# Performance work log

Hardware: AMD Instinct MI355X
Metric: run time of the kernel (lower is better)

Reference implementation:

```python
import math
import jax, jax.numpy as jnp
import numpy as np

B = 2
N = 48           # max_atoms
A = 16           # num_atom_types
E = 5            # num_bond_types
HID = 384
NH = 8
HD = HID // NH   # 48
LYR = 4
MLP = 4 * HID
L = N + N * N    # 2352 sequence length (nodes + flattened edges)


def setup_inputs() -> dict:
    key = jax.random.key(0)
    ks = iter(jax.random.split(key, 48))
    r = lambda *s: jax.random.normal(next(ks), s, jnp.float32) * 0.02
    d = {
        "x": jax.random.normal(next(ks), (B, N, A), jnp.float32),
        "adj": jax.random.normal(next(ks), (B, N, N, E), jnp.float32),
        "t": jax.random.uniform(next(ks), (B,), jnp.float32),
        # embeddings
        "node_w": r(A, HID), "node_b": jnp.zeros((HID,), jnp.float32),
        "edge_w": r(E, HID), "edge_b": jnp.zeros((HID,), jnp.float32),
        "pos": r(L, HID),
        # timestep MLP (SinusoidalPositionalEmbedding(HID) -> Linear(HID,4H) -> SiLU -> Linear(4H,H))
        "t_w1": r(HID, 4 * HID), "t_b1": jnp.zeros((4 * HID,), jnp.float32),
        "t_w2": r(4 * HID, HID), "t_b2": jnp.zeros((HID,), jnp.float32),
        # stacked per-layer params
        "ada1_w": r(LYR, HID, 2 * HID), "ada1_b": jnp.zeros((LYR, 2 * HID), jnp.float32),
        "ada2_w": r(LYR, HID, 2 * HID), "ada2_b": jnp.zeros((LYR, 2 * HID), jnp.float32),
        "q_w": r(LYR, HID, HID), "q_b": jnp.zeros((LYR, HID), jnp.float32),
        "k_w": r(LYR, HID, HID), "k_b": jnp.zeros((LYR, HID), jnp.float32),
        "v_w": r(LYR, HID, HID), "v_b": jnp.zeros((LYR, HID), jnp.float32),
        "o_w": r(LYR, HID, HID), "o_b": jnp.zeros((LYR, HID), jnp.float32),
        "m1_w": r(LYR, HID, MLP), "m1_b": jnp.zeros((LYR, MLP), jnp.float32),
        "m2_w": r(LYR, MLP, HID), "m2_b": jnp.zeros((LYR, HID), jnp.float32),
        # final norm + heads (heads random instead of zero-init so output is informative)
        "fn_g": jnp.ones((HID,), jnp.float32), "fn_b": jnp.zeros((HID,), jnp.float32),
        "on_w": r(HID, A), "on_b": jnp.zeros((A,), jnp.float32),
        "oe_w": r(HID, E), "oe_b": jnp.zeros((E,), jnp.float32),
    }
    return d


def _ln(z):
    # LayerNorm(elementwise_affine=False), eps=1e-5
    mu = z.mean(-1, keepdims=True)
    var = z.var(-1, keepdims=True)
    return (z - mu) * jax.lax.rsqrt(var + 1e-5)


def _forward(x, adj, t, node_w, node_b, edge_w, edge_b, pos,
             t_w1, t_b1, t_w2, t_b2,
             ada1_w, ada1_b, ada2_w, ada2_b,
             q_w, q_b, k_w, k_b, v_w, v_b, o_w, o_b,
             m1_w, m1_b, m2_w, m2_b,
             fn_g, fn_b, on_w, on_b, oe_w, oe_b):
    b = x.shape[0]
    # embed nodes and edges, concat into sequence [b, L, HID]
    h_nodes = x @ node_w + node_b                       # [b, N, H]
    h_edges = adj.reshape(b, N * N, E) @ edge_w + edge_b  # [b, N*N, H]
    h = jnp.concatenate([h_nodes, h_edges], axis=1) + pos[None]
    # sinusoidal timestep embedding -> cond [b, HID]
    half = HID // 2
    freqs = jnp.exp(-math.log(10000.0) * jnp.arange(half, dtype=jnp.float32) / half)
    ang = t[:, None].astype(jnp.float32) * freqs[None, :]
    temb = jnp.concatenate([jnp.sin(ang), jnp.cos(ang)], axis=-1)
    cond = jax.nn.silu(temb @ t_w1 + t_b1) @ t_w2 + t_b2
    inv_scale = 1.0 / math.sqrt(HD)
    for i in range(LYR):
        # AdaLN 1 + attention
        sc, sh = jnp.split(cond @ ada1_w[i] + ada1_b[i], 2, axis=-1)
        n = _ln(h) * (1.0 + sc[:, None, :]) + sh[:, None, :]
        q = (n @ q_w[i] + q_b[i]).reshape(b, L, NH, HD)
        k = (n @ k_w[i] + k_b[i]).reshape(b, L, NH, HD)
        v = (n @ v_w[i] + v_b[i]).reshape(b, L, NH, HD)
        scores = jnp.einsum('bqhd,bkhd->bhqk', q, k) * inv_scale
        attn = jax.nn.softmax(scores, axis=-1)
        ao = jnp.einsum('bhqk,bkhd->bqhd', attn, v).reshape(b, L, HID)
        h = h + ao @ o_w[i] + o_b[i]
        # AdaLN 2 + MLP (exact GELU as in nn.GELU default)
        sc2, sh2 = jnp.split(cond @ ada2_w[i] + ada2_b[i], 2, axis=-1)
        n2 = _ln(h) * (1.0 + sc2[:, None, :]) + sh2[:, None, :]
        h = h + jax.nn.gelu(n2 @ m1_w[i] + m1_b[i], approximate=False) @ m2_w[i] + m2_b[i]
    h = _ln(h) * fn_g + fn_b
    node_out = h[:, :N] @ on_w + on_b                   # [b, N, A]
    edge_out = (h[:, N:] @ oe_w + oe_b).reshape(b, N, N, E)
    return node_out, edge_out


def reference(x, adj, t, node_w, node_b, edge_w, edge_b, pos,
              t_w1, t_b1, t_w2, t_b2,
              ada1_w, ada1_b, ada2_w, ada2_b,
              q_w, q_b, k_w, k_b, v_w, v_b, o_w, o_b,
              m1_w, m1_b, m2_w, m2_b,
              fn_g, fn_b, on_w, on_b, oe_w, oe_b):
    return _forward(x, adj, t, node_w, node_b, edge_w, edge_b, pos,
                    t_w1, t_b1, t_w2, t_b2,
                    ada1_w, ada1_b, ada2_w, ada2_b,
                    q_w, q_b, k_w, k_b, v_w, v_b, o_w, o_b,
                    m1_w, m1_b, m2_w, m2_b,
                    fn_g, fn_b, on_w, on_b, oe_w, oe_b)
```

## Files before the change

### kernel.cpp

```cpp
#include <hip/hip_runtime.h>
#include <hip/hip_bf16.h>
#include <math.h>

typedef __hip_bfloat16 bf16;
typedef __attribute__((ext_vector_type(8))) short short8;
typedef __attribute__((ext_vector_type(4))) float f32x4;

#define B_ 2
#define N_ 48
#define A_ 16
#define E_ 5
#define HID 384
#define NHD 8
#define HD 48
#define LYR 4
#define MLPD 1536
#define L_ 2352
#define M_ 4704
#define VLP 2432
#define QSCALE 0.20823513f

#define WQ_  0LL
#define WK_  589824LL
#define WV_  1179648LL
#define WO_  1769472LL
#define WM1_ 2359296LL
#define WM2_ 4718592LL
#define WTOT 7077888
#define BQ_  0
#define BK_  1536
#define BV_  3072
#define BO_  4608
#define BM1_ 6144
#define BM2_ 12288
#define BTOT 13824

#define GLOAD16(gp, lp) __builtin_amdgcn_global_load_lds( \
    (const __attribute__((address_space(1))) unsigned int*)(gp), \
    (__attribute__((address_space(3))) unsigned int*)(lp), 16, 0, 0)

static __device__ __forceinline__ float b2f(bf16 v) { return __bfloat162float(v); }
static __device__ __forceinline__ float us2f(unsigned short u) {
    return __uint_as_float(((unsigned)u) << 16);
}
static __device__ __forceinline__ unsigned short f2us(float f) {
    bf16 h = __float2bfloat16(f);
    return *reinterpret_cast<unsigned short*>(&h);
}
static __device__ __forceinline__ float ldv(const float* p, size_t i) { return p[i]; }
static __device__ __forceinline__ float ldv(const bf16*  p, size_t i) { return b2f(p[i]); }
static __device__ __forceinline__ void  stv(float* p, size_t i, float v) { p[i] = v; }
static __device__ __forceinline__ void  stv(bf16*  p, size_t i, float v) { p[i] = __float2bfloat16(v); }
static __device__ __forceinline__ float4 ld4(const float* p, size_t i) {
    return *reinterpret_cast<const float4*>(p + i);
}
static __device__ __forceinline__ float4 ld4(const bf16* p, size_t i) {
    ushort4 u = *reinterpret_cast<const ushort4*>(p + i);
    return make_float4(us2f(u.x), us2f(u.y), us2f(u.z), us2f(u.w));
}

__global__ void k_detect(const void* w, int* flag) {
    if (threadIdx.x == 0 && blockIdx.x == 0) {
        const bf16* p = (const bf16*)w;
        int isf = 0;
        for (int i = 0; i < 256; ++i) {
            float v = fabsf(b2f(p[i]));
            if (!(v <= 1000.0f)) { isf = 1; break; }
        }
        *flag = isf;
    }
}

template <typename T>
static __device__ void prepw_body(
    const T* q_w, const T* k_w, const T* v_w, const T* o_w,
    const T* m1_w, const T* m2_w, bf16* wbt)
{
    __shared__ unsigned short Ts[64][72];
    const int z = blockIdx.y;
    const int kind = z >> 2, l = z & 3;
    const T* src; int K, N; long long dbase;
    switch (kind) {
        case 0: src = q_w;  K = 384;  N = 384;  dbase = WQ_;  break;
        case 1: src = k_w;  K = 384;  N = 384;  dbase = WK_;  break;
        case 2: src = v_w;  K = 384;  N = 384;  dbase = WV_;  break;
        case 3: src = o_w;  K = 384;  N = 384;  dbase = WO_;  break;
        case 4: src = m1_w; K = 384;  N = 1536; dbase = WM1_; break;
        default: src = m2_w; K = 1536; N = 384; dbase = WM2_; break;
    }
    const int Nt = N >> 6;
    const int tiles = (K >> 6) * Nt;
    if (blockIdx.x >= tiles) return;
    const int tk = blockIdx.x / Nt, tn = blockIdx.x % Nt;
    const int k0 = tk*64, n0 = tn*64;
    const size_t soff = (size_t)l * K * N;
    const size_t doff = (size_t)dbase + (size_t)l * K * N;
    const int tid = threadIdx.x;
    {
        const int kk = tid >> 2, nc = (tid & 3) * 16;
        #pragma unroll
        for (int j = 0; j < 16; ++j)
            Ts[kk][nc + j] = f2us(ldv(src, soff + (size_t)(k0 + kk)*N + n0 + nc + j));
    }
    __syncthreads();
    {
        const int nn = tid >> 2, kc = (tid & 3) * 16;
        unsigned short tmp[16];
        #pragma unroll
        for (int j = 0; j < 16; ++j) tmp[j] = Ts[kc + j][nn];
        unsigned short* dst = (unsigned short*)wbt + doff + (size_t)(n0 + nn)*K + k0 + kc;
        *reinterpret_cast<short8*>(dst)     = *reinterpret_cast<short8*>(&tmp[0]);
        *reinterpret_cast<short8*>(dst + 8) = *reinterpret_cast<short8*>(&tmp[8]);
    }
}

__global__ __launch_bounds__(256) void k_prepw(
    const void* q_w, const void* k_w, const void* v_w, const void* o_w,
    const void* m1_w, const void* m2_w, const int* __restrict__ fl, bf16* __restrict__ wbt)
{
    if (*fl) prepw_body<float>((const float*)q_w, (const float*)k_w, (const float*)v_w,
                               (const float*)o_w, (const float*)m1_w, (const float*)m2_w, wbt);
    else     prepw_body<bf16>((const bf16*)q_w, (const bf16*)k_w, (const bf16*)v_w,
                              (const bf16*)o_w, (const bf16*)m1_w, (const bf16*)m2_w, wbt);
}

template <typename T>
static __device__ void prepb_body(
    const T* q_b, const T* k_b, const T* v_b, const T* o_b,
    const T* m1_b, const T* m2_b, bf16* bb)
{
    for (int i = threadIdx.x; i < BTOT; i += 256) {
        float v;
        if      (i < BK_)  v = ldv(q_b,  i);
        else if (i < BV_)  v = ldv(k_b,  i - BK_);
        else if (i < BO_)  v = ldv(v_b,  i - BV_);
        else if (i < BM1_) v = ldv(o_b,  i - BO_);
        else if (i < BM2_) v = ldv(m1_b, i - BM1_);
        else               v = ldv(m2_b, i - BM2_);
        bb[i] = __float2bfloat16(v);
    }
}

__global__ __launch_bounds__(256) void k_prepb(
    const void* q_b, const void* k_b, const void* v_b, const void* o_b,
    const void* m1_b, const void* m2_b, const int* __restrict__ fl, bf16* __restrict__ bb)
{
    if (*fl) prepb_body<float>((const float*)q_b, (const float*)k_b, (const float*)v_b,
                               (const float*)o_b, (const float*)m1_b, (const float*)m2_b, bb);
    else     prepb_body<bf16>((const bf16*)q_b, (const bf16*)k_b, (const bf16*)v_b,
                              (const bf16*)o_b, (const bf16*)m1_b, (const bf16*)m2_b, bb);
}

template <typename T>
static __device__ void embed_body(
    const T* x, const T* adj, const T* node_w, const T* node_b,
    const T* edge_w, const T* edge_b, const T* pos, float* h)
{
    const int bl = blockIdx.x;
    const int b = bl / L_, l = bl % L_;
    const int c = threadIdx.x;
    float acc;
    if (l < N_) {
        acc = ldv(node_b, c);
        const size_t xr = (size_t)(b*N_ + l)*A_;
        #pragma unroll
        for (int a = 0; a < A_; ++a) acc += ldv(x, xr + a) * ldv(node_w, (size_t)a*HID + c);
    } else {
        const int e = l - N_;
        acc = ldv(edge_b, c);
        const size_t ar = ((size_t)b*N_*N_ + e)*E_;
        #pragma unroll
        for (int j = 0; j < E_; ++j) acc += ldv(adj, ar + j) * ldv(edge_w, (size_t)j*HID + c);
    }
    h[(size_t)bl*HID + c] = acc + ldv(pos, (size_t)l*HID + c);
}

__global__ __launch_bounds__(384) void k_embed(
    const void* x, const void* adj, const void* node_w, const void* node_b,
    const void* edge_w, const void* edge_b, const void* pos,
    const int* __restrict__ fl, float* __restrict__ h)
{
    if (*fl) embed_body<float>((const float*)x, (const float*)adj, (const float*)node_w,
                               (const float*)node_b, (const float*)edge_w, (const float*)edge_b,
                               (const float*)pos, h);
    else     embed_body<bf16>((const bf16*)x, (const bf16*)adj, (const bf16*)node_w,
                              (const bf16*)node_b, (const bf16*)edge_w, (const bf16*)edge_b,
                              (const bf16*)pos, h);
}

template <typename T>
static __device__ void cond1_body(const T* t, const T* t_w1, const T* t_b1, float* hid)
{
    __shared__ float temb[HID];
    __shared__ float red[4][64];
    const int b = blockIdx.x, jb = blockIdx.y, tid = threadIdx.x;
    const float tv = ldv(t, b);
    for (int c = tid; c < HID; c += 256) {
        int i = (c < 192) ? c : c - 192;
        float f = expf(-9.2103403719761836f * (float)i / 192.0f);
        float ang = tv * f;
        temb[c] = (c < 192) ? sinf(ang) : cosf(ang);
    }
    __syncthreads();
    const int ko = tid >> 6, jo = tid & 63;
    const int j = jb*64 + jo;
    float acc = 0.f;
    for (int i = ko*96; i < (ko + 1)*96; ++i)
        acc += temb[i] * ldv(t_w1, (size_t)i*4*HID + j);
    red[ko][jo] = acc;
    __syncthreads();
    if (ko == 0) {
        float a = red[0][jo] + red[1][jo] + red[2][jo] + red[3][jo] + ldv(t_b1, j);
        hid[(size_t)b*4*HID + j] = a / (1.0f + expf(-a));
    }
}

__global__ __launch_bounds__(256) void k_cond1(
    const void* t, const void* t_w1, const void* t_b1,
    const int* __restrict__ fl, float* __restrict__ hid)
{
    if (*fl) cond1_body<float>((const float*)t, (const float*)t_w1, (const float*)t_b1, hid);
    else     cond1_body<bf16>((const bf16*)t, (const bf16*)t_w1, (const bf16*)t_b1, hid);
}

template <typename T>
static __device__ void cond2_body(const T* t_w2, const T* t_b2, const float* hid, float* part)
{
    __shared__ float hs[128];
    const int b = blockIdx.x, ch = blockIdx.y, c = threadIdx.x;
    const int j0 = ch*128;
    if (c < 128) hs[c] = hid[(size_t)b*4*HID + j0 + c];
    __syncthreads();
    float acc = (ch == 0) ? ldv(t_b2, c) : 0.f;
    for (int jj = 0; jj < 128; ++jj)
        acc += hs[jj] * ldv(t_w2, (size_t)(j0 + jj)*HID + c);
    part[((size_t)b*12 + ch)*HID + c] = acc;
}

__global__ __launch_bounds__(384) void k_cond2(
    const void* t_w2, const void* t_b2, const int* __restrict__ fl,
    const float* __restrict__ hid, float* __restrict__ part)
{
    if (*fl) cond2_body<float>((const float*)t_w2, (const float*)t_b2, hid, part);
    else     cond2_body<bf16>((const bf16*)t_w2, (const bf16*)t_b2, hid, part);
}

template <typename T>
static __device__ void cond3_body(
    const T* ada1_w, const T* ada1_b, const T* ada2_w, const T* ada2_b,
    const float* part, float* ada_out)
{
    __shared__ float cs[HID];
    const int slot = blockIdx.x / 3, ob = blockIdx.x % 3, b = blockIdx.y;
    const int tid = threadIdx.x;
    for (int c = tid; c < HID; c += 256) {
        float s = 0.f;
        #pragma unroll
        for (int ch = 0; ch < 12; ++ch) s += part[((size_t)b*12 + ch)*HID + c];
        cs[c] = s;
    }
    __syncthreads();
    const int layer = slot >> 1, which = slot & 1;
    const int o = ob*256 + tid;
    const T* W  = which ? ada2_w : ada1_w;
    const T* Bi = which ? ada2_b : ada1_b;
    float acc = ldv(Bi, (size_t)layer*768 + o);
    const size_t wb = (size_t)layer*HID*768 + o;
    for (int c = 0; c < HID; ++c) acc += cs[c] * ldv(W, wb + (size_t)c*768);
    ada_out[((size_t)slot*B_ + b)*768 + o] = acc;
}

__global__ __launch_bounds__(256) void k_cond3(
    const void* ada1_w, const void* ada1_b, const void* ada2_w, const void* ada2_b,
    const int* __restrict__ fl, const float* __restrict__ part, float* __restrict__ ada_out)
{
    if (*fl) cond3_body<float>((const float*)ada1_w, (const float*)ada1_b,
                               (const float*)ada2_w, (const float*)ada2_b, part, ada_out);
    else     cond3_body<bf16>((const bf16*)ada1_w, (const bf16*)ada1_b,
                              (const bf16*)ada2_w, (const bf16*)ada2_b, part, ada_out);
}

__global__ __launch_bounds__(256) void k_adaln(
    const float* __restrict__ h, const float* __restrict__ ada,
    bf16* __restrict__ n, int slot)
{
    const int row  = blockIdx.x * 4 + (threadIdx.x >> 6);
    const int lane = threadIdx.x & 63;
    const int b = row / L_;
    const float* hr = h + (size_t)row*HID;
    float v[6]; float s = 0.f, ss = 0.f;
    #pragma unroll
    for (int j = 0; j < 6; ++j) { float t = hr[lane + j*64]; v[j] = t; s += t; ss += t*t; }
    #pragma unroll
    for (int off = 32; off; off >>= 1) { s += __shfl_xor(s, off); ss += __shfl_xor(ss, off); }
    const float mu = s * (1.0f/HID);
    const float rs = rsqrtf(fmaxf(ss * (1.0f/HID) - mu*mu, 0.0f) + 1e-5f);
    const float* ap = ada + ((size_t)slot*B_ + b)*768;
    bf16* nr = n + (size_t)row*HID;
    #pragma unroll
    for (int j = 0; j < 6; ++j) {
        int c = lane + j*64;
        nr[c] = __float2bfloat16((v[j] - mu)*rs*(1.0f + ap[c]) + ap[384 + c]);
    }
}

static __device__ __forceinline__ void gemm_epilogue(
    f32x4 (&acc)[2][2], float bcol0, float bcol1,
    bf16* Cb, float* Cf, int M, int N, int act, int mode,
    int bm, int bn, int wm, int wn, int quad, int c)
{
    const float bcol[2] = {bcol0, bcol1};
    #pragma unroll
    for (int mi = 0; mi < 2; ++mi)
        #pragma unroll
        for (int ni = 0; ni < 2; ++ni) {
            const int col = bn + wn*32 + ni*16 + c;
            #pragma unroll
            for (int r = 0; r < 4; ++r) {
                const int row = bm + wm*32 + mi*16 + quad*4 + r;
                if (row < M) {
                    float v = acc[mi][ni][r] + bcol[ni];
                    if (act) v = 0.5f * v * (1.0f + erff(v * 0.70710678118654752f));
                    if (mode == 1) Cf[(size_t)row*N + col] += v;
                    else if (mode == 0) Cb[(size_t)row*N + col] = __float2bfloat16(v);
                    else if (mode == 3) Cb[(size_t)row*N + col] = __float2bfloat16(v * QSCALE);
                    else {
                        const int b   = row >= L_ ? 1 : 0;
                        const int key = row - b*L_;
                        const int hh  = col / 48, d = col - hh*48;
                        Cb[((size_t)(b*8 + hh)*48 + d)*VLP + key] = __float2bfloat16(v);
                    }
                }
            }
        }
}

template <typename T>
static __device__ void gemm_body(
    const bf16* A, const T* W, long long woff, const T* bias, long long boff,
    bf16* Cb, float* Cf, int M, int N, int K, int act, int mode)
{
    __shared__ __align__(16) unsigned short As[64][72];
    __shared__ __align__(16) unsigned short Bt[64][72];
    const int tid  = threadIdx.x;
    const int wv   = tid >> 6, lane = tid & 63;
    const int quad = lane >> 4, c = lane & 15;
    const int wm = wv & 1, wn = wv >> 1;
    const int bm = blockIdx.x * 64, bn = blockIdx.y * 64;
    const int arow = tid >> 3, ach = tid & 7;
    f32x4 acc[2][2] = {{{0.f,0.f,0.f,0.f},{0.f,0.f,0.f,0.f}},
                       {{0.f,0.f,0.f,0.f},{0.f,0.f,0.f,0.f}}};
    for (int k0 = 0; k0 < K; k0 += 64) {
        short8 av[2]; float4 w0[2], w1[2];
        #pragma unroll
        for (int i = 0; i < 2; ++i) {
            const int row = i*32 + arow;
            av[i] = short8{0,0,0,0,0,0,0,0};
            if (bm + row < M)
                av[i] = *reinterpret_cast<const short8*>(
                            A + (size_t)(bm + row)*K + k0 + ach*8);
            const size_t wrow = (size_t)woff + (size_t)(k0 + i*32 + arow)*N + bn + ach*8;
            w0[i] = ld4(W, wrow);
            w1[i] = ld4(W, wrow + 4);
        }
        __syncthreads();
        #pragma unroll
        for (int i = 0; i < 2; ++i) {
            *reinterpret_cast<short8*>(&As[i*32 + arow][ach*8]) = av[i];
            const int kk = i*32 + arow, nb0 = ach*8;
            Bt[nb0+0][kk] = f2us(w0[i].x); Bt[nb0+1][kk] = f2us(w0[i].y);
            Bt[nb0+2][kk] = f2us(w0[i].z); Bt[nb0+3][kk] = f2us(w0[i].w);
            Bt[nb0+4][kk] = f2us(w1[i].x); Bt[nb0+5][kk] = f2us(w1[i].y);
            Bt[nb0+6][kk] = f2us(w1[i].z); Bt[nb0+7][kk] = f2us(w1[i].w);
        }
        __syncthreads();
        #pragma unroll
        for (int ks = 0; ks < 2; ++ks) {
            short8 af[2], bfr[2];
            #pragma unroll
            for (int mi = 0; mi < 2; ++mi)
                af[mi] = *reinterpret_cast<const short8*>(
                             &As[wm*32 + mi*16 + c][ks*32 + quad*8]);
            #pragma unroll
            for (int ni = 0; ni < 2; ++ni)
                bfr[ni] = *reinterpret_cast<const short8*>(
                              &Bt[wn*32 + ni*16 + c][ks*32 + quad*8]);
            #pragma unroll
            for (int mi = 0; mi < 2; ++mi)
                #pragma unroll
                for (int ni = 0; ni < 2; ++ni)
                    acc[mi][ni] = __builtin_amdgcn_mfma_f32_16x16x32_bf16(
                                      af[mi], bfr[ni], acc[mi][ni], 0, 0, 0);
        }
    }
    gemm_epilogue(acc, ldv(bias, (size_t)boff + bn + wn*32 + c),
                  ldv(bias, (size_t)boff + bn + wn*32 + 16 + c),
                  Cb, Cf, M, N, act, mode, bm, bn, wm, wn, quad, c);
}

__global__ __launch_bounds__(256) void k_gemm(
    const bf16* __restrict__ A, const void* W, long long woff, const void* bias, long long boff,
    bf16* Cb, float* Cf, int M, int N, int K, int act, int mode,
    const int* __restrict__ fl)
{
    if (*fl) gemm_body<float>(A, (const float*)W, woff, (const float*)bias, boff,
                              Cb, Cf, M, N, K, act, mode);
    else     gemm_body<bf16>(A, (const bf16*)W, woff, (const bf16*)bias, boff,
                             Cb, Cf, M, N, K, act, mode);
}

__global__ __launch_bounds__(256) void k_gemm_qkv(
    const bf16* __restrict__ A,
    const void* qw, const void* kw, const void* vw,
    const void* qb, const void* kb, const void* vb,
    long long woff, long long boff,
    bf16* Cq, bf16* Ck, bf16* Cv, const int* __restrict__ fl)
{
    const int z = blockIdx.z;
    const void* W  = (z == 0) ? qw : (z == 1) ? kw : vw;
    const void* Bi = (z == 0) ? qb : (z == 1) ? kb : vb;
    bf16* C        = (z == 0) ? Cq : (z == 1) ? Ck : Cv;
    const int mode = (z == 0) ? 3 : (z == 2) ? 2 : 0;
    if (*fl) gemm_body<float>(A, (const float*)W, woff, (const float*)Bi, boff,
                              C, nullptr, M_, HID, HID, 0, mode);
    else     gemm_body<bf16>(A, (const bf16*)W, woff, (const bf16*)Bi, boff,
                             C, nullptr, M_, HID, HID, 0, mode);
}

static __device__ void gemm_t_body(
    const bf16* A, const bf16* Wt, long long woff, const bf16* bias, long long boff,
    bf16* Cb, float* Cf, int M, int N, int K, int act, int mode)
{
    __shared__ __align__(16) unsigned short Tz[2][2][4096];
    const int tid  = threadIdx.x;
    const int wv   = tid >> 6, lane = tid & 63;
    const int quad = lane >> 4, c = lane & 15;
    const int wm = wv & 1, wn = wv >> 1;
    const int bm = blockIdx.x * 64, bn = blockIdx.y * 64;
    const unsigned short* Ag = (const unsigned short*)A;
    const unsigned short* Wg = (const unsigned short*)Wt + woff;
    const int sr = tid >> 3;
    const int csw0 = (((tid & 7) ^ (sr & 7)) << 3);
    int ar0 = bm + sr;        ar0 = ar0 < M ? ar0 : M - 1;
    int ar1 = bm + 32 + sr;   ar1 = ar1 < M ? ar1 : M - 1;
    const int wr0 = bn + sr, wr1 = bn + 32 + sr;
    const int ldso = tid * 8;

    f32x4 acc[2][2] = {{{0.f,0.f,0.f,0.f},{0.f,0.f,0.f,0.f}},
                       {{0.f,0.f,0.f,0.f},{0.f,0.f,0.f,0.f}}};

    #define STAGE_T(buf, k0) do { \
        GLOAD16(Ag + (size_t)ar0*K + (k0) + csw0, &Tz[buf][0][ldso]); \
        GLOAD16(Ag + (size_t)ar1*K + (k0) + csw0, &Tz[buf][0][2048 + ldso]); \
        GLOAD16(Wg + (size_t)wr0*K + (k0) + csw0, &Tz[buf][1][ldso]); \
        GLOAD16(Wg + (size_t)wr1*K + (k0) + csw0, &Tz[buf][1][2048 + ldso]); \
    } while (0)

    STAGE_T(0, 0);
    __syncthreads();
    int cur = 0;
    for (int k0 = 0; k0 < K; k0 += 64) {
        if (k0 + 64 < K) STAGE_T(cur ^ 1, k0 + 64);
        #pragma unroll
        for (int ks = 0; ks < 2; ++ks) {
            short8 af[2], bfr[2];
            #pragma unroll
            for (int mi = 0; mi < 2; ++mi) {
                const int row = wm*32 + mi*16 + c;
                const char* p = (const char*)&Tz[cur][0][0]
                              + (row*128 + (((ks*64 + quad*16)) ^ ((row & 7) << 4)));
                af[mi] = *reinterpret_cast<const short8*>(p);
            }
            #pragma unroll
            for (int ni = 0; ni < 2; ++ni) {
                const int row = wn*32 + ni*16 + c;
                const char* p = (const char*)&Tz[cur][1][0]
                              + (row*128 + (((ks*64 + quad*16)) ^ ((row & 7) << 4)));
                bfr[ni] = *reinterpret_cast<const short8*>(p);
            }
            #pragma unroll
            for (int mi = 0; mi < 2; ++mi)
                #pragma unroll
                for (int ni = 0; ni < 2; ++ni)
                    acc[mi][ni] = __builtin_amdgcn_mfma_f32_16x16x32_bf16(
                                      af[mi], bfr[ni], acc[mi][ni], 0, 0, 0);
        }
        __syncthreads();
        cur ^= 1;
    }
    #undef STAGE_T
    gemm_epilogue(acc, b2f(bias[boff + bn + wn*32 + c]),
                  b2f(bias[boff + bn + wn*32 + 16 + c]),
                  Cb, Cf, M, N, act, mode, bm, bn, wm, wn, quad, c);
}

__global__ __launch_bounds__(256) void k_gemm_t(
    const bf16* __restrict__ A, const bf16* __restrict__ Wt, long long woff,
    const bf16* __restrict__ bias, long long boff,
    bf16* Cb, float* Cf, int M, int N, int K, int act, int mode)
{
    gemm_t_body(A, Wt, woff, bias, boff, Cb, Cf, M, N, K, act, mode);
}

__global__ __launch_bounds__(256) void k_gemm_qkv_t(
    const bf16* __restrict__ A, const bf16* __restrict__ wbt, const bf16* __restrict__ bb,
    int lyr, bf16* Cq, bf16* Ck, bf16* Cv)
{
    const int z = blockIdx.z;
    long long woff; long long boff; bf16* C; int mode;
    if (z == 0)      { woff = WQ_ + (long long)lyr*147456; boff = BQ_ + lyr*384; C = Cq; mode = 3; }
    else if (z == 1) { woff = WK_ + (long long)lyr*147456; boff = BK_ + lyr*384; C = Ck; mode = 0; }
    else             { woff = WV_ + (long long)lyr*147456; boff = BV_ + lyr*384; C = Cv; mode = 2; }
    gemm_t_body(A, wbt, woff, bb, boff, C, nullptr, M_, HID, HID, 0, mode);
}

__global__ __launch_bounds__(512) void k_attn(
    const bf16* __restrict__ q, const bf16* __restrict__ k,
    const bf16* __restrict__ vt, bf16* __restrict__ ao)
{
    __shared__ __align__(16) unsigned short Ks[2][64][80];
    __shared__ __align__(16) unsigned short Vt[2][48][72];
    __shared__ __align__(16) unsigned short Pq[8][16][72];
    const int tid  = threadIdx.x;
    const int w    = tid >> 6, lane = tid & 63;
    const int quad = lane >> 4, c = lane & 15;
    const int qt = w & 3, sp = w >> 2;
    const int bh = blockIdx.y;
    const size_t base  = (size_t)(bh >> 3)*L_*HID + (size_t)(bh & 7)*HD;
    const size_t vbase = (size_t)bh*48*VLP;
    const int q0 = blockIdx.x*64 + qt*16;
    const bool qvalid = q0 < L_;
    const int qrow = qvalid ? (q0 + c) : c;

    short8 qf0, qf1;
    {
        const unsigned short* qp = (const unsigned short*)(q + base + (size_t)qrow*HID);
        qf0 = *reinterpret_cast<const short8*>(qp + quad*8);
        if (quad < 2) qf1 = *reinterpret_cast<const short8*>(qp + 32 + quad*8);
        else          qf1 = short8{0,0,0,0,0,0,0,0};
    }
    f32x4 o0 = {0.f,0.f,0.f,0.f}, o1 = {0.f,0.f,0.f,0.f}, o2 = {0.f,0.f,0.f,0.f};
    float m = -3.0e38f, lsum = 0.f;

    const int t256 = tid & 255, grp = tid >> 8;
    const int krow0 = t256 >> 3, kch = t256 & 7;
    const int krow1 = 32 + krow0;
    const int vd0 = krow0;
    const int vd1 = 32 + (krow0 & 15);
    const bool vl1 = (t256 < 128);
    const unsigned short* kq = (const unsigned short*)(k + base);
    const unsigned short* vq = (const unsigned short*)(vt + vbase);
    const short8 Z8 = short8{0,0,0,0,0,0,0,0};
    short8 kr0 = Z8, kr1 = Z8, vr0, vr1 = Z8;
    {
        const int kb0 = grp*1216;
        if (kch < 6) {
            kr0 = *reinterpret_cast<const short8*>(kq + (size_t)(kb0 + krow0)*HID + kch*8);
            kr1 = *reinterpret_cast<const short8*>(kq + (size_t)(kb0 + krow1)*HID + kch*8);
        }
        vr0 = *reinterpret_cast<const short8*>(vq + (size_t)vd0*VLP + kb0 + kch*8);
        if (vl1) vr1 = *reinterpret_cast<const short8*>(vq + (size_t)vd1*VLP + kb0 + kch*8);
    }

    for (int tt = 0; tt < 19; ++tt) {
        __syncthreads();
        *reinterpret_cast<short8*>(&Ks[grp][krow0][kch*8]) = kr0;
        *reinterpret_cast<short8*>(&Ks[grp][krow1][kch*8]) = kr1;
        *reinterpret_cast<short8*>(&Vt[grp][vd0][kch*8])   = vr0;
        if (vl1) *reinterpret_cast<short8*>(&Vt[grp][vd1][kch*8]) = vr1;
        __syncthreads();
        if (tt < 18) {
            const int nb0 = grp*1216 + (tt + 1)*64;
            if (kch < 6) {
                kr0 = *reinterpret_cast<const short8*>(kq + (size_t)(nb0 + krow0)*HID + kch*8);
                kr1 = *reinterpret_cast<const short8*>(kq + (size_t)(nb0 + krow1)*HID + kch*8);
            }
            vr0 = *reinterpret_cast<const short8*>(vq + (size_t)vd0*VLP + nb0 + kch*8);
            if (vl1) vr1 = *reinterpret_cast<const short8*>(vq + (size_t)vd1*VLP + nb0 + kch*8);
        }

        const int kt = sp*1216 + tt*64;
        float sv[16];
        #pragma unroll
        for (int t = 0; t < 4; ++t) {
            f32x4 acc = {0.f,0.f,0.f,0.f};
            short8 a0 = *reinterpret_cast<const short8*>(&Ks[sp][t*16 + c][quad*8]);
            short8 a1 = *reinterpret_cast<const short8*>(&Ks[sp][t*16 + c][32 + quad*8]);
            acc = __builtin_amdgcn_mfma_f32_16x16x32_bf16(a0, qf0, acc, 0, 0, 0);
            acc = __builtin_amdgcn_mfma_f32_16x16x32_bf16(a1, qf1, acc, 0, 0, 0);
            #pragma unroll
            for (int r = 0; r < 4; ++r) sv[t*4 + r] = acc[r];
        }
        if (sp == 1 && tt >= 17) {
            #pragma unroll
            for (int t = 0; t < 4; ++t)
                #pragma unroll
                for (int r = 0; r < 4; ++r)
                    if (kt + t*16 + quad*4 + r >= L_) sv[t*4 + r] = -3.0e38f;
        }
        float tmax = fmaxf(fmaxf(fmaxf(sv[0], sv[1]),  fmaxf(sv[2],  sv[3])),
                           fmaxf(fmaxf(sv[4], sv[5]),  fmaxf(sv[6],  sv[7])));
        float tmx2 = fmaxf(fmaxf(fmaxf(sv[8], sv[9]),  fmaxf(sv[10], sv[11])),
                           fmaxf(fmaxf(sv[12], sv[13]), fmaxf(sv[14], sv[15])));
        tmax = fmaxf(tmax, tmx2);
        tmax = fmaxf(tmax, __shfl_xor(tmax, 16));
        tmax = fmaxf(tmax, __shfl_xor(tmax, 32));
        if (!__all(tmax <= m + 8.0f)) {
            const float mn = fmaxf(m, tmax);
            const float alpha = exp2f(m - mn);
            m = mn;
            lsum *= alpha;
            o0 *= alpha; o1 *= alpha; o2 *= alpha;
        }
        float psum = 0.f;
        unsigned short pv[16];
        #pragma unroll
        for (int i = 0; i < 16; ++i) {
            const float p = exp2f(sv[i] - m);
            psum += p;
            pv[i] = f2us(p);
        }
        lsum += psum;
        #pragma unroll
        for (int t = 0; t < 4; ++t)
            *reinterpret_cast<ushort4*>(&Pq[w][c][t*16 + quad*4]) =
                make_ushort4(pv[t*4+0], pv[t*4+1], pv[t*4+2], pv[t*4+3]);
        #pragma unroll
        for (int s = 0; s < 2; ++s) {
            short8 pf  = *reinterpret_cast<const short8*>(&Pq[w][c][s*32 + quad*8]);
            short8 vf0 = *reinterpret_cast<const short8*>(&Vt[sp][c][s*32 + quad*8]);
            short8 vf1 = *reinterpret_cast<const short8*>(&Vt[sp][16 + c][s*32 + quad*8]);
            short8 vf2 = *reinterpret_cast<const short8*>(&Vt[sp][32 + c][s*32 + quad*8]);
            o0 = __builtin_amdgcn_mfma_f32_16x16x32_bf16(vf0, pf, o0, 0, 0, 0);
            o1 = __builtin_amdgcn_mfma_f32_16x16x32_bf16(vf1, pf, o1, 0, 0, 0);
            o2 = __builtin_amdgcn_mfma_f32_16x16x32_bf16(vf2, pf, o2, 0, 0, 0);
        }
    }
    float lw = lsum;
    lw += __shfl_xor(lw, 16);
    lw += __shfl_xor(lw, 32);
    float* Mg = (float*)&Ks[0][0][0];
    __syncthreads();
    if (sp == 1) {
        float* dst = Mg + (size_t)(qt*64 + lane)*14;
        dst[0] = o0[0]; dst[1] = o0[1]; dst[2]  = o0[2]; dst[3]  = o0[3];
        dst[4] = o1[0]; dst[5] = o1[1]; dst[6]  = o1[2]; dst[7]  = o1[3];
        dst[8] = o2[0]; dst[9] = o2[1]; dst[10] = o2[2]; dst[11] = o2[3];
        dst[12] = m; dst[13] = lw;
    }
    __syncthreads();
    if (sp == 0 && qvalid) {
        const float* src = Mg + (size_t)(qt*64 + lane)*14;
        const float m2 = src[12], l2 = src[13];
        const float mm = fmaxf(m, m2);
        const float a1 = exp2f(m - mm), a2 = exp2f(m2 - mm);
        const float inv = 1.0f / (lw*a1 + l2*a2);
        unsigned short* orow = (unsigned short*)(ao + base + (size_t)(q0 + c)*HID);
        const f32x4 ot[3] = {o0, o1, o2};
        #pragma unroll
        for (int dt = 0; dt < 3; ++dt) {
            ushort4 w4;
            w4.x = f2us((ot[dt][0]*a1 + src[dt*4+0]*a2) * inv);
            w4.y = f2us((ot[dt][1]*a1 + src[dt*4+1]*a2) * inv);
            w4.z = f2us((ot[dt][2]*a1 + src[dt*4+2]*a2) * inv);
            w4.w = f2us((ot[dt][3]*a1 + src[dt*4+3]*a2) * inv);
            *reinterpret_cast<ushort4*>(orow + dt*16 + quad*4) = w4;
        }
    }
}

template <typename T, typename TO>
static __device__ void final_body(
    const float* h, const T* fn_g, const T* fn_b,
    const T* on_w, const T* on_b, const T* oe_w, const T* oe_b, TO* out)
{
    __shared__ float hf[HID];
    const int row = blockIdx.x;
    const int b = row / L_, l = row % L_;
    const int lane = threadIdx.x;
    const float* hr = h + (size_t)row*HID;
    float v[6]; float s = 0.f, ss = 0.f;
    #pragma unroll
    for (int j = 0; j < 6; ++j) { float t = hr[lane + j*64]; v[j] = t; s += t; ss += t*t; }
    #pragma unroll
    for (int off = 32; off; off >>= 1) { s += __shfl_xor(s, off); ss += __shfl_xor(ss, off); }
    const float mu = s * (1.0f/HID);
    const float rs = rsqrtf(fmaxf(ss * (1.0f/HID) - mu*mu, 0.0f) + 1e-5f);
    #pragma unroll
    for (int j = 0; j < 6; ++j) {
        int c = lane + j*64;
        hf[c] = (v[j] - mu) * rs * ldv(fn_g, c) + ldv(fn_b, c);
    }
    __syncthreads();
    if (l < N_) {
        if (lane < A_) {
            float acc = ldv(on_b, lane);
            for (int c = 0; c < HID; ++c) acc += hf[c] * ldv(on_w, (size_t)c*A_ + lane);
            stv(out, (size_t)(b*N_ + l)*A_ + lane, acc);
        }
    } else {
        const int e = l - N_;
        if (lane < E_) {
            float acc = ldv(oe_b, lane);
            for (int c = 0; c < HID; ++c) acc += hf[c] * ldv(oe_w, (size_t)c*E_ + lane);
            stv(out, (size_t)B_*N_*A_ + ((size_t)b*N_*N_ + e)*E_ + lane, acc);
        }
    }
}

__global__ __launch_bounds__(64) void k_final(
    const float* __restrict__ h, const void* fn_g, const void* fn_b,
    const void* on_w, const void* on_b, const void* oe_w, const void* oe_b,
    const int* __restrict__ fl, void* out)
{
    if (*fl) final_body<float, float>(h, (const float*)fn_g, (const float*)fn_b,
                                      (const float*)on_w, (const float*)on_b,
                                      (const float*)oe_w, (const float*)oe_b, (float*)out);
    else     final_body<bf16, bf16>(h, (const bf16*)fn_g, (const bf16*)fn_b,
                                    (const bf16*)on_w, (const bf16*)on_b,
                                    (const bf16*)oe_w, (const bf16*)oe_b, (bf16*)out);
}

extern "C" void kernel_launch(void* const* d_in, const int* in_sizes, int n_in,
                              void* d_out, int out_size, void* d_ws, size_t ws_size,
                              hipStream_t stream) {
    const void* x      = d_in[0];
    const void* adj    = d_in[1];
    const void* t      = d_in[2];
    const void* node_w = d_in[3];
    const void* node_b = d_in[4];
    const void* edge_w = d_in[5];
    const void* edge_b = d_in[6];
    const void* pos    = d_in[7];
    const void* t_w1   = d_in[8];
    const void* t_b1   = d_in[9];
    const void* t_w2   = d_in[10];
    const void* t_b2   = d_in[11];
    const void* ada1_w = d_in[12];
    const void* ada1_b = d_in[13];
    const void* ada2_w = d_in[14];
    const void* ada2_b = d_in[15];
    const void* q_w    = d_in[16];
    const void* q_b    = d_in[17];
    const void* k_w    = d_in[18];
    const void* k_b    = d_in[19];
    const void* v_w    = d_in[20];
    const void* v_b    = d_in[21];
    const void* o_w    = d_in[22];
    const void* o_b    = d_in[23];
    const void* m1_w   = d_in[24];
    const void* m1_b   = d_in[25];
    const void* m2_w   = d_in[26];
    const void* m2_b   = d_in[27];
    const void* fn_g   = d_in[28];
    const void* fn_b   = d_in[29];
    const void* on_w   = d_in[30];
    const void* on_b   = d_in[31];
    const void* oe_w   = d_in[32];
    const void* oe_b   = d_in[33];

    const size_t SZ  = (size_t)M_ * HID;
    const size_t VTZ = (size_t)B_*NHD*HD*VLP;
    const size_t FLT = SZ + 12288 + (size_t)B_*4*HID + (size_t)B_*12*HID;
    const size_t M1FULL = (size_t)M_ * MLPD;
    const size_t BF_BASE = 3*SZ + VTZ;
    const size_t BF_BIG  = SZ + M1FULL;
    const size_t NEED      = 256 + sizeof(float)*FLT + sizeof(bf16)*BF_BASE;
    const size_t NEED_BIG  = 256 + sizeof(float)*FLT + sizeof(bf16)*BF_BIG;
    const size_t NEED_PREP = 256 + sizeof(float)*FLT
                           + sizeof(bf16)*(BF_BIG + WTOT + BTOT);
    if (ws_size < NEED) {
        hipMemsetAsync(d_out, 0, (size_t)out_size*sizeof(bf16), stream);
        return;
    }
    const bool big  = (ws_size >= NEED_BIG);
    const bool prep = (ws_size >= NEED_PREP);
    int*   fl   = (int*)d_ws;
    float* h    = (float*)((char*)d_ws + 256);
    float* ada  = h + SZ;
    float* hid  = ada + 12288;
    float* part = hid + (size_t)B_*4*HID;
    bf16* nb  = (bf16*)(part + (size_t)B_*12*HID);
    bf16* qb  = nb + SZ;
    bf16* kb  = qb + SZ;
    bf16* vtb = kb + SZ;
    bf16* m1c = kb;
    bf16* m1f = qb;
    bf16* wbt = nb + BF_BIG;
    bf16* bb  = wbt + WTOT;

    k_detect<<<1, 64, 0, stream>>>(node_w, fl);
    if (prep) {
        k_prepw<<<dim3(144, 24), 256, 0, stream>>>(q_w, k_w, v_w, o_w, m1_w, m2_w, fl, wbt);
        k_prepb<<<1, 256, 0, stream>>>(q_b, k_b, v_b, o_b, m1_b, m2_b, fl, bb);
    }
    k_embed<<<M_, HID, 0, stream>>>(x, adj, node_w, node_b, edge_w, edge_b, pos, fl, h);
    k_cond1<<<dim3(B_, 24), 256, 0, stream>>>(t, t_w1, t_b1, fl, hid);
    k_cond2<<<dim3(B_, 12), 384, 0, stream>>>(t_w2, t_b2, fl, hid, part);
    k_cond3<<<dim3(24, B_), 256, 0, stream>>>(ada1_w, ada1_b, ada2_w, ada2_b, fl, part, ada);
    for (int i = 0; i < LYR; ++i) {
        const long long woff   = (long long)i * HID * HID;
        const long long boff   = (long long)i * HID;
        const long long m1woff = (long long)i * HID * MLPD;
        const long long m1boff = (long long)i * MLPD;
        const long long m2woff = (long long)i * MLPD * HID;

        k_adaln<<<M_/4, 256, 0, stream>>>(h, ada, nb, 2*i);
        if (prep) {
            k_gemm_qkv_t<<<dim3(74, 6, 3), 256, 0, stream>>>(nb, wbt, bb, i, qb, kb, vtb);
            k_attn<<<dim3(37, B_*NHD), 512, 0, stream>>>(qb, kb, vtb, nb);
            k_gemm_t<<<dim3(74, 6), 256, 0, stream>>>(nb, wbt, WO_ + (long long)i*147456,
                                                      bb, BO_ + i*384,
                                                      nullptr, h, M_, HID, HID, 0, 1);
            k_adaln<<<M_/4, 256, 0, stream>>>(h, ada, nb, 2*i + 1);
            k_gemm_t<<<dim3(74, 24), 256, 0, stream>>>(nb, wbt, WM1_ + (long long)i*589824,
                                                       bb, BM1_ + i*MLPD,
                                                       m1f, nullptr, M_, MLPD, HID, 1, 0);
            k_gemm_t<<<dim3(74, 6), 256, 0, stream>>>(m1f, wbt, WM2_ + (long long)i*589824,
                                                      bb, BM2_ + i*384,
                                                      nullptr, h, M_, HID, MLPD, 0, 1);
        } else {
            k_gemm_qkv<<<dim3(74, 6, 3), 256, 0, stream>>>(nb, q_w, k_w, v_w, q_b, k_b, v_b,
                                                           woff, boff, qb, kb, vtb, fl);
            k_attn<<<dim3(37, B_*NHD), 512, 0, stream>>>(qb, kb, vtb, nb);
            k_gemm<<<dim3(74, 6), 256, 0, stream>>>(nb, o_w, woff, o_b, boff,
                                                    nullptr, h, M_, HID, HID, 0, 1, fl);
            k_adaln<<<M_/4, 256, 0, stream>>>(h, ada, nb, 2*i + 1);
            if (big) {
                k_gemm<<<dim3(74, 24), 256, 0, stream>>>(nb, m1_w, m1woff, m1_b, m1boff,
                                                         m1f, nullptr, M_, MLPD, HID, 1, 0, fl);
                k_gemm<<<dim3(74, 6), 256, 0, stream>>>(m1f, m2_w, m2woff, m2_b, boff,
                                                        nullptr, h, M_, HID, MLPD, 0, 1, fl);
            } else {
                for (int c = 0; c < 2; ++c) {
                    k_gemm<<<dim3(37, 24), 256, 0, stream>>>(nb + (size_t)c*2352*HID,
                                                             m1_w, m1woff, m1_b, m1boff,
                                                             m1c, nullptr, 2352, MLPD, HID, 1, 0, fl);
                    k_gemm<<<dim3(37, 6), 256, 0, stream>>>(m1c, m2_w, m2woff, m2_b, boff,
                                                            nullptr, h + (size_t)c*2352*HID,
                                                            2352, HID, MLPD, 0, 1, fl);
                }
            }
        }
    }
    k_final<<<M_, 64, 0, stream>>>(h, fn_g, fn_b, on_w, on_b, oe_w, oe_b, fl, (void*)d_out);
}
```

Measured before the change: 818.1 us.

## Split attention keys across two blocks with flash-decoding style merge kernel

Adds a split-K attention kernel where each block handles half of the key sequence with 256 threads, writing normalized partial outputs plus max/sum stats to workspace, and a separate merge kernel that combines the two halves. This replaces the in-block two-wave split with grid-level splitting, doubling block count for better CU occupancy. It costs extra global writes/reads of partials and an extra kernel launch, and only runs if the workspace is large enough.

```diff
diff --git a/kernel.cpp b/kernel.cpp
--- a/kernel.cpp
+++ b/kernel.cpp
@@ -34,6 +34,9 @@
 #define BM1_ 6144
 #define BM2_ 12288
 #define BTOT 13824
+
+#define PO_E  ((size_t)16*2368*2*48)
+#define PML_E ((size_t)16*2368*2*2)
 
 #define GLOAD16(gp, lp) __builtin_amdgcn_global_load_lds( \
     (const __attribute__((address_space(1))) unsigned int*)(gp), \
@@ -666,6 +669,174 @@
             w4.w = f2us((ot[dt][3]*a1 + src[dt*4+3]*a2) * inv);
             *reinterpret_cast<ushort4*>(orow + dt*16 + quad*4) = w4;
         }
+    }
+}
+
+__global__ __launch_bounds__(256) void k_attn_fd(
+    const bf16* __restrict__ q, const bf16* __restrict__ k,
+    const bf16* __restrict__ vt, bf16* __restrict__ pob, float* __restrict__ pml)
+{
+    __shared__ __align__(16) unsigned short Ks[64][80];
+    __shared__ __align__(16) unsigned short Vt[48][72];
+    __shared__ __align__(16) unsigned short Pq[4][16][72];
+    const int tid  = threadIdx.x;
+    const int w    = tid >> 6, lane = tid & 63;
+    const int quad = lane >> 4, c = lane & 15;
+    const int bh   = blockIdx.y;
+    const int half = blockIdx.z;
+    const size_t base  = (size_t)(bh >> 3)*L_*HID + (size_t)(bh & 7)*HD;
+    const size_t vbase = (size_t)bh*48*VLP;
+    const int q0 = blockIdx.x*64 + w*16;
+    const bool qvalid = q0 < L_;
+    const int qrow = qvalid ? (q0 + c) : c;
+
+    short8 qf0, qf1;
+    {
+        const unsigned short* qp = (const unsigned short*)(q + base + (size_t)qrow*HID);
+        qf0 = *reinterpret_cast<const short8*>(qp + quad*8);
+        if (quad < 2) qf1 = *reinterpret_cast<const short8*>(qp + 32 + quad*8);
+        else          qf1 = short8{0,0,0,0,0,0,0,0};
+    }
+    f32x4 o0 = {0.f,0.f,0.f,0.f}, o1 = {0.f,0.f,0.f,0.f}, o2 = {0.f,0.f,0.f,0.f};
+    float m = -3.0e38f, lsum = 0.f;
+
+    const int krow0 = tid >> 3, kch = tid & 7;
+    const int krow1 = 32 + krow0;
+    const int vd0 = krow0;
+    const int vd1 = 32 + (krow0 & 15);
+    const bool vl1 = (tid < 128);
+    const unsigned short* kq = (const unsigned short*)(k + base);
+    const unsigned short* vq = (const unsigned short*)(vt + vbase);
+    const short8 Z8 = short8{0,0,0,0,0,0,0,0};
+    short8 kr0 = Z8, kr1 = Z8, vr0, vr1 = Z8;
+    const int kbase = half*1216;
+    {
+        if (kch < 6) {
+            kr0 = *reinterpret_cast<const short8*>(kq + (size_t)(kbase + krow0)*HID + kch*8);
+            kr1 = *reinterpret_cast<const short8*>(kq + (size_t)(kbase + krow1)*HID + kch*8);
+        }
+        vr0 = *reinterpret_cast<const short8*>(vq + (size_t)vd0*VLP + kbase + kch*8);
+        if (vl1) vr1 = *reinterpret_cast<const short8*>(vq + (size_t)vd1*VLP + kbase + kch*8);
+    }
+
+    for (int tt = 0; tt < 19; ++tt) {
+        __syncthreads();
+        *reinterpret_cast<short8*>(&Ks[krow0][kch*8]) = kr0;
+        *reinterpret_cast<short8*>(&Ks[krow1][kch*8]) = kr1;
+        *reinterpret_cast<short8*>(&Vt[vd0][kch*8])   = vr0;
+        if (vl1) *reinterpret_cast<short8*>(&Vt[vd1][kch*8]) = vr1;
+        __syncthreads();
+        if (tt < 18) {
+            const int nb0 = kbase + (tt + 1)*64;
+            if (kch < 6) {
+                kr0 = *reinterpret_cast<const short8*>(kq + (size_t)(nb0 + krow0)*HID + kch*8);
+                kr1 = *reinterpret_cast<const short8*>(kq + (size_t)(nb0 + krow1)*HID + kch*8);
+            }
+            vr0 = *reinterpret_cast<const short8*>(vq + (size_t)vd0*VLP + nb0 + kch*8);
+            if (vl1) vr1 = *reinterpret_cast<const short8*>(vq + (size_t)vd1*VLP + nb0 + kch*8);
+        }
+
+        const int kt = kbase + tt*64;
+        float sv[16];
+        #pragma unroll
+        for (int t = 0; t < 4; ++t) {
+            f32x4 acc = {0.f,0.f,0.f,0.f};
+            short8 a0 = *reinterpret_cast<const short8*>(&Ks[t*16 + c][quad*8]);
+            short8 a1 = *reinterpret_cast<const short8*>(&Ks[t*16 + c][32 + quad*8]);
+            acc = __builtin_amdgcn_mfma_f32_16x16x32_bf16(a0, qf0, acc, 0, 0, 0);
+            acc = __builtin_amdgcn_mfma_f32_16x16x32_bf16(a1, qf1, acc, 0, 0, 0);
+            #pragma unroll
+            for (int r = 0; r < 4; ++r) sv[t*4 + r] = acc[r];
+        }
+        if (half == 1 && tt >= 17) {
+            #pragma unroll
+            for (int t = 0; t < 4; ++t)
+                #pragma unroll
+                for (int r = 0; r < 4; ++r)
+                    if (kt + t*16 + quad*4 + r >= L_) sv[t*4 + r] = -3.0e38f;
+        }
+        float tmax = fmaxf(fmaxf(fmaxf(sv[0], sv[1]),  fmaxf(sv[2],  sv[3])),
+                           fmaxf(fmaxf(sv[4], sv[5]),  fmaxf(sv[6],  sv[7])));
+        float tmx2 = fmaxf(fmaxf(fmaxf(sv[8], sv[9]),  fmaxf(sv[10], sv[11])),
+                           fmaxf(fmaxf(sv[12], sv[13]), fmaxf(sv[14], sv[15])));
+        tmax = fmaxf(tmax, tmx2);
+        tmax = fmaxf(tmax, __shfl_xor(tmax, 16));
+        tmax = fmaxf(tmax, __shfl_xor(tmax, 32));
+        if (!__all(tmax <= m + 8.0f)) {
+            const float mn = fmaxf(m, tmax);
+            const float alpha = exp2f(m - mn);
+            m = mn;
+            lsum *= alpha;
+            o0 *= alpha; o1 *= alpha; o2 *= alpha;
+        }
+        float psum = 0.f;
+        unsigned short pv[16];
+        #pragma unroll
+        for (int i = 0; i < 16; ++i) {
+            const float p = exp2f(sv[i] - m);
+            psum += p;
+            pv[i] = f2us(p);
+        }
+        lsum += psum;
+        #pragma unroll
+        for (int t = 0; t < 4; ++t)
+            *reinterpret_cast<ushort4*>(&Pq[w][c][t*16 + quad*4]) =
+                make_ushort4(pv[t*4+0], pv[t*4+1], pv[t*4+2], pv[t*4+3]);
+        #pragma unroll
+        for (int s = 0; s < 2; ++s) {
+            short8 pf  = *reinterpret_cast<const short8*>(&Pq[w][c][s*32 + quad*8]);
+            short8 vf0 = *reinterpret_cast<const short8*>(&Vt[c][s*32 + quad*8]);
+            short8 vf1 = *reinterpret_cast<const short8*>(&Vt[16 + c][s*32 + quad*8]);
+            short8 vf2 = *reinterpret_cast<const short8*>(&Vt[32 + c][s*32 + quad*8]);
+            o0 = __builtin_amdgcn_mfma_f32_16x16x32_bf16(vf0, pf, o0, 0, 0, 0);
+            o1 = __builtin_amdgcn_mfma_f32_16x16x32_bf16(vf1, pf, o1, 0, 0, 0);
+            o2 = __builtin_amdgcn_mfma_f32_16x16x32_bf16(vf2, pf, o2, 0, 0, 0);
+        }
+    }
+    float lw = lsum;
+    lw += __shfl_xor(lw, 16);
+    lw += __shfl_xor(lw, 32);
+    const float invl = 1.0f / lw;
+    const size_t ro = ((size_t)bh*2368 + q0 + c)*2 + half;
+    unsigned short* pr = (unsigned short*)pob + ro*48;
+    const f32x4 ot[3] = {o0, o1, o2};
+    #pragma unroll
+    for (int dt = 0; dt < 3; ++dt) {
+        ushort4 w4;
+        w4.x = f2us(ot[dt][0]*invl);
+        w4.y = f2us(ot[dt][1]*invl);
+        w4.z = f2us(ot[dt][2]*invl);
+        w4.w = f2us(ot[dt][3]*invl);
+        *reinterpret_cast<ushort4*>(pr + dt*16 + quad*4) = w4;
+    }
+    if (quad == 0) { pml[ro*2 + 0] = m; pml[ro*2 + 1] = lw; }
+}
+
+__global__ __launch_bounds__(256) void k_amerge(
+    const bf16* __restrict__ pob, const float* __restrict__ pml, bf16* __restrict__ ao)
+{
+    const int tid = threadIdx.x;
+    const int bh = blockIdx.y;
+    const int qq = blockIdx.x*16 + (tid >> 4);
+    const int j = tid & 15;
+    const size_t ro = ((size_t)bh*2368 + qq)*2;
+    const float m1 = pml[ro*2 + 0], l1 = pml[ro*2 + 1];
+    const float m2 = pml[ro*2 + 2], l2 = pml[ro*2 + 3];
+    const float mm = fmaxf(m1, m2);
+    const float b1 = exp2f(m1 - mm)*l1, b2 = exp2f(m2 - mm)*l2;
+    const float inv = 1.0f / (b1 + b2);
+    const float w1 = b1*inv, w2 = b2*inv;
+    if (j < 12) {
+        const unsigned short* p1 = (const unsigned short*)pob + ro*48 + j*4;
+        ushort4 u1 = *reinterpret_cast<const ushort4*>(p1);
+        ushort4 u2 = *reinterpret_cast<const ushort4*>(p1 + 48);
+        ushort4 o4;
+        o4.x = f2us(us2f(u1.x)*w1 + us2f(u2.x)*w2);
+        o4.y = f2us(us2f(u1.y)*w1 + us2f(u2.y)*w2);
+        o4.z = f2us(us2f(u1.z)*w1 + us2f(u2.z)*w2);
+        o4.w = f2us(us2f(u1.w)*w1 + us2f(u2.w)*w2);
+        const size_t base = (size_t)(bh >> 3)*L_*HID + (size_t)(bh & 7)*HD;
+        *reinterpret_cast<ushort4*>((unsigned short*)ao + base + (size_t)qq*HID + j*4) = o4;
     }
 }
 
@@ -769,12 +940,14 @@
     const size_t NEED_BIG  = 256 + sizeof(float)*FLT + sizeof(bf16)*BF_BIG;
     const size_t NEED_PREP = 256 + sizeof(float)*FLT
                            + sizeof(bf16)*(BF_BIG + WTOT + BTOT);
+    const size_t NEED_FD   = NEED_PREP + sizeof(bf16)*PO_E + sizeof(float)*PML_E;
     if (ws_size < NEED) {
         hipMemsetAsync(d_out, 0, (size_t)out_size*sizeof(bf16), stream);
         return;
     }
     const bool big  = (ws_size >= NEED_BIG);
     const bool prep = (ws_size >= NEED_PREP);
+    const bool fd   = (ws_size >= NEED_FD);
     int*   fl   = (int*)d_ws;
     float* h    = (float*)((char*)d_ws + 256);
     float* ada  = h + SZ;
@@ -788,6 +961,8 @@
     bf16* m1f = qb;
     bf16* wbt = nb + BF_BIG;
     bf16* bb  = wbt + WTOT;
+    bf16* pob = bb + BTOT;
+    float* pml = (float*)(pob + PO_E);
 
     k_detect<<<1, 64, 0, stream>>>(node_w, fl);
     if (prep) {
@@ -808,7 +983,12 @@
         k_adaln<<<M_/4, 256, 0, stream>>>(h, ada, nb, 2*i);
         if (prep) {
             k_gemm_qkv_t<<<dim3(74, 6, 3), 256, 0, stream>>>(nb, wbt, bb, i, qb, kb, vtb);
-            k_attn<<<dim3(37, B_*NHD), 512, 0, stream>>>(qb, kb, vtb, nb);
+            if (fd) {
+                k_attn_fd<<<dim3(37, 16, 2), 256, 0, stream>>>(qb, kb, vtb, pob, pml);
+                k_amerge<<<dim3(147, 16), 256, 0, stream>>>(pob, pml, nb);
+            } else {
+                k_attn<<<dim3(37, B_*NHD), 512, 0, stream>>>(qb, kb, vtb, nb);
+            }
             k_gemm_t<<<dim3(74, 6), 256, 0, stream>>>(nb, wbt, WO_ + (long long)i*147456,
                                                       bb, BO_ + i*384,
                                                       nullptr, h, M_, HID, HID, 0, 1);
```

Measured after the change: 811.4 us. About the same (-0.8%).
